# Optimization experiments

Measured on AMD Instinct MI355X. Metric: run time of the kernel, lower is better.

## Reference

```python
import jax, jax.numpy as jnp
import numpy as np
import math

DIM = 1024
NUM_HEADS = 16
HEAD_DIM = DIM // NUM_HEADS  # 64
BATCH = 4
SEQ = 4096


def setup_inputs() -> dict:
    key = jax.random.key(0)
    ks = jax.random.split(key, 10)
    s = 1.0 / math.sqrt(DIM)
    return {
        "x": jax.random.normal(ks[0], (BATCH, SEQ, DIM), dtype=jnp.float32),
        "Wq": jax.random.normal(ks[1], (DIM, DIM), dtype=jnp.float32) * s,
        "bq": jax.random.normal(ks[2], (DIM,), dtype=jnp.float32) * 0.01,
        "Wk": jax.random.normal(ks[3], (DIM, DIM), dtype=jnp.float32) * s,
        "bk": jax.random.normal(ks[4], (DIM,), dtype=jnp.float32) * 0.01,
        "Wv": jax.random.normal(ks[5], (DIM, DIM), dtype=jnp.float32) * s,
        "bv": jax.random.normal(ks[6], (DIM,), dtype=jnp.float32) * 0.01,
        "Wo": jax.random.normal(ks[7], (DIM, DIM), dtype=jnp.float32) * s,
        "bo": jax.random.normal(ks[8], (DIM,), dtype=jnp.float32) * 0.01,
        # Performer random projection buffer: randn * 0.4, [head_dim, feature_map_size]
        "R": jax.random.normal(ks[9], (HEAD_DIM, HEAD_DIM), dtype=jnp.float32) * 0.4,
    }


def _feature_map(x, R):
    # x: [b, h, n, d]; matches torch: x scaled first, then norm of scaled x
    x = x / math.sqrt(HEAD_DIM)
    proj = jnp.einsum("bhnd,dm->bhnm", x, R)
    sq_norm = jnp.sum(x * x, axis=-1, keepdims=True)  # ||x||^2
    return jnp.exp(proj - 0.5 * sq_norm)


def reference(x, Wq, bq, Wk, bk, Wv, bv, Wo, bo, R):
    b, n, _ = x.shape
    h, d = NUM_HEADS, HEAD_DIM

    def split_heads(t):
        return t.reshape(b, n, h, d).transpose(0, 2, 1, 3)  # [b,h,n,d]

    q = split_heads(x @ Wq.T + bq)
    k = split_heads(x @ Wk.T + bk)
    v = split_heads(x @ Wv.T + bv)

    q_prime = _feature_map(q, R)  # [b,h,n,m]
    k_prime = _feature_map(k, R)  # [b,h,n,m]

    kv = jnp.einsum("bhnd,bhne->bhde", k_prime, v)          # [b,h,m,d]
    z = 1.0 / (jnp.sum(q_prime, axis=-1) + 1e-8)            # [b,h,n]
    out = jnp.einsum("bhnd,bhde,bhn->bhne", q_prime, kv, z)  # [b,h,n,d]

    out = out.transpose(0, 2, 1, 3).reshape(b, n, DIM)
    return out @ Wo.T + bo
```

## Files before the change

### kernel.cpp

```cpp
#include <hip/hip_runtime.h>
#include <math.h>

#define DIM 1024
#define NH 16
#define HD 64
#define BATCH 4
#define SEQ 4096
#define NTOK (BATCH*SEQ)

typedef float f32x4 __attribute__((ext_vector_type(4)));
typedef short bf16x8 __attribute__((ext_vector_type(8)));

#define GLOAD_LDS16(gp, lp)                                                    \
  __builtin_amdgcn_global_load_lds(                                            \
      (const __attribute__((address_space(1))) unsigned int*)(gp),             \
      (__attribute__((address_space(3))) unsigned int*)(lp), 16, 0, 0)

__device__ __forceinline__ unsigned short f2bf(float f) {
  unsigned u = __float_as_uint(f);
  unsigned r = (u + 0x7fffu + ((u >> 16) & 1u)) >> 16;
  return (unsigned short)r;
}
__device__ __forceinline__ float bf2f(unsigned short s) {
  return __uint_as_float((unsigned)s << 16);
}

template <int NB_N, int OUT_BF16>
__global__ __launch_bounds__(256) void gemm_swz(
    const unsigned short* __restrict__ A,
    const unsigned short* __restrict__ B,
    const float* __restrict__ b0, const float* __restrict__ b1,
    const float* __restrict__ b2,
    void* __restrict__ C0, void* __restrict__ C1, void* __restrict__ C2)
{
    __shared__ unsigned short As[128 * 32];
    __shared__ unsigned short Bs[128 * 32];
    const int t    = threadIdx.x;
    const int lane = t & 63;
    const int w    = t >> 6;

    const int bid   = blockIdx.x;
    const int xcd   = bid & 7;
    const int local = bid >> 3;
    const int mi    = xcd * 16 + local / NB_N;
    const int ni    = local % NB_N;
    const int m0    = mi * 128;
    const int n0g   = ni * 128;

    const int wm = (w >> 1) * 64;
    const int wn = (w & 1) * 64;

    f32x4 acc[4][4] = {};

    const int srow = lane >> 2;
    const int sseg = ((lane & 3) ^ ((lane >> 3) & 3)) * 8;

    const int fr = lane & 15;
    const int q8 = lane >> 4;
    const int fq = (q8 ^ ((fr >> 1) & 3)) * 8;

    for (int k0 = 0; k0 < 1024; k0 += 32) {
#pragma unroll
        for (int i = 0; i < 2; i++) {
            int rbase = i * 64 + w * 16;
            GLOAD_LDS16(&A[(size_t)(m0 + rbase + srow) * 1024 + k0 + sseg],
                        &As[rbase * 32]);
            GLOAD_LDS16(&B[(size_t)(n0g + rbase + srow) * 1024 + k0 + sseg],
                        &Bs[rbase * 32]);
        }
        __syncthreads();

        bf16x8 af[4], bfr[4];
#pragma unroll
        for (int mt = 0; mt < 4; mt++)
            af[mt] = *(const bf16x8*)&As[(wm + mt * 16 + fr) * 32 + fq];
#pragma unroll
        for (int nt = 0; nt < 4; nt++)
            bfr[nt] = *(const bf16x8*)&Bs[(wn + nt * 16 + fr) * 32 + fq];
#pragma unroll
        for (int mt = 0; mt < 4; mt++)
#pragma unroll
            for (int nt = 0; nt < 4; nt++)
                acc[mt][nt] = __builtin_amdgcn_mfma_f32_16x16x32_bf16(
                    af[mt], bfr[nt], acc[mt][nt], 0, 0, 0);
        __syncthreads();
    }

    const int mat = ni >> 3;
    const float* bias = (NB_N == 8) ? b0 : (mat == 0 ? b0 : mat == 1 ? b1 : b2);
    void* Cp = (NB_N == 8) ? C0 : (mat == 0 ? C0 : mat == 1 ? C1 : C2);
    const int n0 = (ni & 7) * 128;

    const int col = lane & 15;
    const int rq  = (lane >> 4) * 4;
#pragma unroll
    for (int nt = 0; nt < 4; nt++) {
        int cbase = n0 + wn + nt * 16 + col;
        float bv = bias[cbase];
#pragma unroll
        for (int mt = 0; mt < 4; mt++) {
#pragma unroll
            for (int r = 0; r < 4; r++) {
                int row = m0 + wm + mt * 16 + rq + r;
                float val = acc[mt][nt][r] + bv;
                if (OUT_BF16)
                    ((unsigned short*)Cp)[(size_t)row * 1024 + cbase] = f2bf(val);
                else
                    ((float*)Cp)[(size_t)row * 1024 + cbase] = val;
            }
        }
    }
}

__global__ __launch_bounds__(256) void cast_bf16(
    const float* __restrict__ src, unsigned short* __restrict__ dst, int n)
{
    int i = (blockIdx.x * 256 + threadIdx.x) * 4;
    if (i >= n) return;
    float4 v = *(const float4*)&src[i];
    ushort2 lo = {f2bf(v.x), f2bf(v.y)};
    ushort2 hi = {f2bf(v.z), f2bf(v.w)};
    *(ushort2*)&dst[i] = lo;
    *(ushort2*)&dst[i + 2] = hi;
}

__global__ __launch_bounds__(256) void cast_bf16_w4(
    const float* __restrict__ s0, const float* __restrict__ s1,
    const float* __restrict__ s2, const float* __restrict__ s3,
    unsigned short* __restrict__ d0, unsigned short* __restrict__ d1,
    unsigned short* __restrict__ d2, unsigned short* __restrict__ d3)
{
    const float* s = (blockIdx.y == 0) ? s0 : (blockIdx.y == 1) ? s1
                    : (blockIdx.y == 2) ? s2 : s3;
    unsigned short* d = (blockIdx.y == 0) ? d0 : (blockIdx.y == 1) ? d1
                       : (blockIdx.y == 2) ? d2 : d3;
    int i = (blockIdx.x * 256 + threadIdx.x) * 4;
    float4 v = *(const float4*)&s[i];
    ushort2 lo = {f2bf(v.x), f2bf(v.y)};
    ushort2 hi = {f2bf(v.z), f2bf(v.w)};
    *(ushort2*)&d[i] = lo;
    *(ushort2*)&d[i + 2] = hi;
}

__global__ __launch_bounds__(256) void featmap_mfma(
    unsigned short* __restrict__ buf, const float* __restrict__ R)
{
    __shared__ unsigned short Rt[64 * 72];
    const int t = threadIdx.x;
    for (int i = t; i < 4096; i += 256) {
        int n = i >> 6, k = i & 63;
        Rt[n * 72 + k] = f2bf(R[k * 64 + n]);
    }
    __syncthreads();

    const int lane = t & 63;
    const int w = t >> 6;
    const size_t rowbase = (size_t)blockIdx.x * 256 + w * 64;
    const int fr = lane & 15;
    const int fq = (lane >> 4) * 8;

    f32x4 acc[4][4] = {};
    float sqacc[4] = {0.f, 0.f, 0.f, 0.f};

#pragma unroll
    for (int ks = 0; ks < 2; ks++) {
        bf16x8 bfr[4];
#pragma unroll
        for (int nt = 0; nt < 4; nt++)
            bfr[nt] = *(const bf16x8*)&Rt[(nt * 16 + fr) * 72 + ks * 32 + fq];
#pragma unroll
        for (int mt = 0; mt < 4; mt++) {
            bf16x8 a = *(const bf16x8*)
                &buf[(rowbase + mt * 16 + fr) * 64 + ks * 32 + fq];
#pragma unroll
            for (int j = 0; j < 8; j++) {
                float v = bf2f((unsigned short)a[j]);
                sqacc[mt] = fmaf(v, v, sqacc[mt]);
            }
#pragma unroll
            for (int nt = 0; nt < 4; nt++)
                acc[mt][nt] = __builtin_amdgcn_mfma_f32_16x16x32_bf16(
                    a, bfr[nt], acc[mt][nt], 0, 0, 0);
        }
    }
#pragma unroll
    for (int mt = 0; mt < 4; mt++) {
        sqacc[mt] += __shfl_xor(sqacc[mt], 16);
        sqacc[mt] += __shfl_xor(sqacc[mt], 32);
    }

    const int col = lane & 15;
    const int rq  = (lane >> 4) * 4;
#pragma unroll
    for (int mt = 0; mt < 4; mt++) {
#pragma unroll
        for (int r = 0; r < 4; r++) {
            float s = __shfl(sqacc[mt], rq + r);
            size_t row = rowbase + mt * 16 + rq + r;
#pragma unroll
            for (int nt = 0; nt < 4; nt++) {
                float val = acc[mt][nt][r] * 0.125f - s * 0.0078125f;
                buf[row * 64 + nt * 16 + col] = f2bf(__expf(val));
            }
        }
    }
}

__global__ __launch_bounds__(256) void kv_accum(
    const unsigned short* __restrict__ kp, const unsigned short* __restrict__ vp,
    float* __restrict__ kv)
{
    __shared__ float Ks[16][68];
    __shared__ float Vs[16][68];
    const int chunk = blockIdx.x;
    const int h = blockIdx.y;
    const int b = blockIdx.z;
    const int t = threadIdx.x;
    const int tx = t & 15, ty = t >> 4;
    float c[4][4] = {};
    const int nbase = b * SEQ + chunk * 512;
    const int nl = t >> 4, seg = t & 15;
    for (int n0 = 0; n0 < 512; n0 += 16) {
        size_t gaddr = (size_t)(nbase + n0 + nl) * DIM + h * 64 + seg * 4;
        ushort4 kq = *(const ushort4*)&kp[gaddr];
        ushort4 vq = *(const ushort4*)&vp[gaddr];
        Ks[nl][seg * 4 + 0] = bf2f(kq.x); Ks[nl][seg * 4 + 1] = bf2f(kq.y);
        Ks[nl][seg * 4 + 2] = bf2f(kq.z); Ks[nl][seg * 4 + 3] = bf2f(kq.w);
        Vs[nl][seg * 4 + 0] = bf2f(vq.x); Vs[nl][seg * 4 + 1] = bf2f(vq.y);
        Vs[nl][seg * 4 + 2] = bf2f(vq.z); Vs[nl][seg * 4 + 3] = bf2f(vq.w);
        __syncthreads();
#pragma unroll
        for (int nn = 0; nn < 16; nn++) {
            float4 a = *(const float4*)&Ks[nn][ty * 4];
            float4 bq = *(const float4*)&Vs[nn][tx * 4];
            float aa[4] = {a.x, a.y, a.z, a.w};
            float bb[4] = {bq.x, bq.y, bq.z, bq.w};
#pragma unroll
            for (int i = 0; i < 4; i++)
#pragma unroll
                for (int j = 0; j < 4; j++)
                    c[i][j] += aa[i] * bb[j];
        }
        __syncthreads();
    }
    float* dst = &kv[(size_t)(b * NH + h) * 64 * 64];
#pragma unroll
    for (int i = 0; i < 4; i++)
#pragma unroll
        for (int j = 0; j < 4; j++)
            atomicAdd(&dst[(ty * 4 + i) * 64 + tx * 4 + j], c[i][j]);
}

__global__ __launch_bounds__(256) void attn_out_mfma(
    const unsigned short* __restrict__ qp, const float* __restrict__ kv,
    unsigned short* __restrict__ ob)
{
    __shared__ unsigned short kvT[64 * 72];
    const int t = threadIdx.x;
    const int bh = blockIdx.y;
    const int b = bh >> 4, h = bh & 15;
    const float* kvp = &kv[(size_t)bh * 4096];
    for (int i = t; i < 4096; i += 256) {
        int m = i >> 6, e = i & 63;
        kvT[e * 72 + m] = f2bf(kvp[i]);
    }
    __syncthreads();

    const int lane = t & 63;
    const int w = t >> 6;
    const int rowInSeq = blockIdx.x * 256 + w * 64;
    const int fr = lane & 15;
    const int fq = (lane >> 4) * 8;

    f32x4 acc[4][4] = {};
    float rsum[4] = {0.f, 0.f, 0.f, 0.f};

#pragma unroll
    for (int ks = 0; ks < 2; ks++) {
        bf16x8 bfr[4];
#pragma unroll
        for (int nt = 0; nt < 4; nt++)
            bfr[nt] = *(const bf16x8*)&kvT[(nt * 16 + fr) * 72 + ks * 32 + fq];
#pragma unroll
        for (int mt = 0; mt < 4; mt++) {
            size_t n = (size_t)(b * SEQ + rowInSeq + mt * 16 + fr);
            bf16x8 a = *(const bf16x8*)&qp[n * DIM + h * 64 + ks * 32 + fq];
#pragma unroll
            for (int j = 0; j < 8; j++)
                rsum[mt] += bf2f((unsigned short)a[j]);
#pragma unroll
            for (int nt = 0; nt < 4; nt++)
                acc[mt][nt] = __builtin_amdgcn_mfma_f32_16x16x32_bf16(
                    a, bfr[nt], acc[mt][nt], 0, 0, 0);
        }
    }
#pragma unroll
    for (int mt = 0; mt < 4; mt++) {
        rsum[mt] += __shfl_xor(rsum[mt], 16);
        rsum[mt] += __shfl_xor(rsum[mt], 32);
    }

    const int col = lane & 15;
    const int rq  = (lane >> 4) * 4;
#pragma unroll
    for (int mt = 0; mt < 4; mt++) {
#pragma unroll
        for (int r = 0; r < 4; r++) {
            float s = __shfl(rsum[mt], rq + r);
            float z = 1.f / (s + 1e-8f);
            size_t n = (size_t)(b * SEQ + rowInSeq + mt * 16 + rq + r);
#pragma unroll
            for (int nt = 0; nt < 4; nt++)
                ob[n * DIM + h * 64 + nt * 16 + col] = f2bf(acc[mt][nt][r] * z);
        }
    }
}

extern "C" void kernel_launch(void* const* d_in, const int* in_sizes, int n_in,
                              void* d_out, int out_size, void* d_ws, size_t ws_size,
                              hipStream_t stream) {
    const float* x  = (const float*)d_in[0];
    const float* Wq = (const float*)d_in[1];
    const float* bq = (const float*)d_in[2];
    const float* Wk = (const float*)d_in[3];
    const float* bk = (const float*)d_in[4];
    const float* Wv = (const float*)d_in[5];
    const float* bv = (const float*)d_in[6];
    const float* Wo = (const float*)d_in[7];
    const float* bo = (const float*)d_in[8];
    const float* R  = (const float*)d_in[9];
    float* out = (float*)d_out;

    char* p = (char*)d_ws;
    unsigned short* xb = (unsigned short*)p; p += (size_t)NTOK * DIM * 2;
    unsigned short* qb = (unsigned short*)p; p += (size_t)NTOK * DIM * 2;
    unsigned short* kb = (unsigned short*)p; p += (size_t)NTOK * DIM * 2;
    unsigned short* vb = (unsigned short*)p; p += (size_t)NTOK * DIM * 2;
    float* kvb = (float*)p;                  p += (size_t)BATCH * NH * HD * HD * 4;
    unsigned short* wqkv = (unsigned short*)p; p += (size_t)3 * DIM * DIM * 2;
    unsigned short* wob  = (unsigned short*)p; p += (size_t)DIM * DIM * 2;

    hipMemsetAsync(kvb, 0, (size_t)BATCH * NH * HD * HD * sizeof(float), stream);

    cast_bf16<<<NTOK * DIM / (256 * 4), 256, 0, stream>>>(x, xb, NTOK * DIM);
    cast_bf16_w4<<<dim3(DIM * DIM / (256 * 4), 4), 256, 0, stream>>>(
        Wq, Wk, Wv, Wo,
        wqkv, wqkv + (size_t)DIM * DIM, wqkv + (size_t)2 * DIM * DIM, wob);

    gemm_swz<24, 1><<<3072, 256, 0, stream>>>(
        xb, wqkv, bq, bk, bv, qb, kb, vb);

    featmap_mfma<<<2 * NTOK * NH / 256, 256, 0, stream>>>(qb, R);

    kv_accum<<<dim3(8, NH, BATCH), 256, 0, stream>>>(kb, vb, kvb);

    attn_out_mfma<<<dim3(SEQ / 256, BATCH * NH), 256, 0, stream>>>(qb, kvb, xb);

    gemm_swz<8, 0><<<1024, 256, 0, stream>>>(
        xb, wob, bo, bo, bo, out, out, out);
}
```

Measured before the change: 419.4 us.

## Replace 128x128 GEMM with 256x256 tile, 4-stage async LDS pipeline

Rewrites both projection GEMMs to use 512-thread blocks computing 256x256 tiles, with a four-deep ring of LDS buffers filled by direct global-to-LDS loads issued three k-steps ahead. Barriers, waitcnt and setprio are placed by hand to overlap loads with MFMA work, and the block-index swizzle spreads tiles across XCDs. The goal is more reuse per tile and hidden memory latency; in exchange it uses 128KB of LDS per block, which limits occupancy, and the last GEMM runs as a single wave of blocks.

```diff
diff --git a/kernel.cpp b/kernel.cpp
--- a/kernel.cpp
+++ b/kernel.cpp
@@ -25,88 +25,134 @@
   return __uint_as_float((unsigned)s << 16);
 }
 
-template <int NB_N, int OUT_BF16>
-__global__ __launch_bounds__(256) void gemm_swz(
+template <int NT_N, int OUT_BF16>
+__global__ __launch_bounds__(512, 2) void gemm256(
     const unsigned short* __restrict__ A,
     const unsigned short* __restrict__ B,
     const float* __restrict__ b0, const float* __restrict__ b1,
     const float* __restrict__ b2,
     void* __restrict__ C0, void* __restrict__ C1, void* __restrict__ C2)
 {
-    __shared__ unsigned short As[128 * 32];
-    __shared__ unsigned short Bs[128 * 32];
+    __shared__ unsigned short lds[4][2][8192];
     const int t    = threadIdx.x;
     const int lane = t & 63;
     const int w    = t >> 6;
 
-    const int bid   = blockIdx.x;
-    const int xcd   = bid & 7;
-    const int local = bid >> 3;
-    const int mi    = xcd * 16 + local / NB_N;
-    const int ni    = local % NB_N;
-    const int m0    = mi * 128;
-    const int n0g   = ni * 128;
-
-    const int wm = (w >> 1) * 64;
-    const int wn = (w & 1) * 64;
-
-    f32x4 acc[4][4] = {};
-
-    const int srow = lane >> 2;
-    const int sseg = ((lane & 3) ^ ((lane >> 3) & 3)) * 8;
+    const int cpx = gridDim.x >> 3;
+    const int swz = (blockIdx.x & 7) * cpx + (blockIdx.x >> 3);
+    const int mi  = swz / NT_N;
+    const int ni  = swz % NT_N;
+    const int m0  = mi * 256;
+    const int n0g = ni * 256;
+
+    const int wm = (w >> 2) * 128;
+    const int wn = (w & 3) * 64;
+
+    const int srow = t >> 2;
+    const int sseg = ((t & 3) ^ ((t >> 3) & 3)) * 8;
+    const unsigned short* Ag = A + (size_t)(m0 + srow) * 1024 + sseg;
+    const unsigned short* Bg = B + (size_t)(n0g + srow) * 1024 + sseg;
+    const int ldst = w * 512;
 
     const int fr = lane & 15;
-    const int q8 = lane >> 4;
-    const int fq = (q8 ^ ((fr >> 1) & 3)) * 8;
-
-    for (int k0 = 0; k0 < 1024; k0 += 32) {
-#pragma unroll
-        for (int i = 0; i < 2; i++) {
-            int rbase = i * 64 + w * 16;
-            GLOAD_LDS16(&A[(size_t)(m0 + rbase + srow) * 1024 + k0 + sseg],
-                        &As[rbase * 32]);
-            GLOAD_LDS16(&B[(size_t)(n0g + rbase + srow) * 1024 + k0 + sseg],
-                        &Bs[rbase * 32]);
-        }
-        __syncthreads();
-
-        bf16x8 af[4], bfr[4];
-#pragma unroll
-        for (int mt = 0; mt < 4; mt++)
-            af[mt] = *(const bf16x8*)&As[(wm + mt * 16 + fr) * 32 + fq];
-#pragma unroll
-        for (int nt = 0; nt < 4; nt++)
-            bfr[nt] = *(const bf16x8*)&Bs[(wn + nt * 16 + fr) * 32 + fq];
-#pragma unroll
-        for (int mt = 0; mt < 4; mt++)
-#pragma unroll
-            for (int nt = 0; nt < 4; nt++)
-                acc[mt][nt] = __builtin_amdgcn_mfma_f32_16x16x32_bf16(
-                    af[mt], bfr[nt], acc[mt][nt], 0, 0, 0);
-        __syncthreads();
-    }
-
-    const int mat = ni >> 3;
-    const float* bias = (NB_N == 8) ? b0 : (mat == 0 ? b0 : mat == 1 ? b1 : b2);
-    void* Cp = (NB_N == 8) ? C0 : (mat == 0 ? C0 : mat == 1 ? C1 : C2);
-    const int n0 = (ni & 7) * 128;
+    const int fq = ((lane >> 4) ^ ((fr >> 1) & 3)) * 8;
+
+    f32x4 acc[8][4] = {};
+
+#define STAGE_A(hh, j)                                                        \
+  GLOAD_LDS16(Ag + (size_t)(j) * 131072 + (size_t)(hh) * 32,                  \
+              &lds[(hh) & 3][0][(j) * 4096 + ldst])
+#define STAGE_B(hh, j)                                                        \
+  GLOAD_LDS16(Bg + (size_t)(j) * 131072 + (size_t)(hh) * 32,                  \
+              &lds[(hh) & 3][1][(j) * 4096 + ldst])
+
+#define BOUNDARY(VM)                                                          \
+  asm volatile("s_waitcnt vmcnt(" #VM ")" ::: "memory");                      \
+  __builtin_amdgcn_s_barrier();                                               \
+  asm volatile("" ::: "memory");
+
+#define KHALF(h, DOSTAGE)                                                     \
+  {                                                                           \
+    const unsigned short* As_ = &lds[(h) & 3][0][0];                          \
+    const unsigned short* Bs_ = &lds[(h) & 3][1][0];                          \
+    bf16x8 bfr[4], afr[4];                                                    \
+    if (DOSTAGE) { STAGE_A((h) + 3, 0); STAGE_A((h) + 3, 1); }                \
+    _Pragma("unroll")                                                         \
+    for (int nf = 0; nf < 4; ++nf)                                            \
+      bfr[nf] = *(const bf16x8*)&Bs_[(wn + nf * 16 + fr) * 32 + fq];          \
+    _Pragma("unroll")                                                         \
+    for (int mf = 0; mf < 4; ++mf)                                            \
+      afr[mf] = *(const bf16x8*)&As_[(wm + mf * 16 + fr) * 32 + fq];          \
+    __builtin_amdgcn_s_barrier();                                             \
+    asm volatile("s_waitcnt lgkmcnt(0)" ::: "memory");                        \
+    __builtin_amdgcn_s_setprio(1);                                            \
+    _Pragma("unroll")                                                         \
+    for (int mf = 0; mf < 4; ++mf)                                            \
+      _Pragma("unroll")                                                       \
+      for (int nf = 0; nf < 4; ++nf)                                          \
+        acc[mf][nf] = __builtin_amdgcn_mfma_f32_16x16x32_bf16(                \
+            afr[mf], bfr[nf], acc[mf][nf], 0, 0, 0);                          \
+    __builtin_amdgcn_s_setprio(0);                                            \
+    __builtin_amdgcn_s_barrier();                                             \
+    asm volatile("" ::: "memory");                                            \
+    if (DOSTAGE) { STAGE_B((h) + 3, 0); STAGE_B((h) + 3, 1); }                \
+    _Pragma("unroll")                                                         \
+    for (int mf = 0; mf < 4; ++mf)                                            \
+      afr[mf] = *(const bf16x8*)&As_[(wm + 64 + mf * 16 + fr) * 32 + fq];     \
+    __builtin_amdgcn_s_barrier();                                             \
+    asm volatile("s_waitcnt lgkmcnt(0)" ::: "memory");                        \
+    __builtin_amdgcn_s_setprio(1);                                            \
+    _Pragma("unroll")                                                         \
+    for (int mf = 0; mf < 4; ++mf)                                            \
+      _Pragma("unroll")                                                       \
+      for (int nf = 0; nf < 4; ++nf)                                          \
+        acc[4 + mf][nf] = __builtin_amdgcn_mfma_f32_16x16x32_bf16(            \
+            afr[mf], bfr[nf], acc[4 + mf][nf], 0, 0, 0);                      \
+    __builtin_amdgcn_s_setprio(0);                                            \
+  }
+
+#pragma unroll
+    for (int hh = 0; hh < 3; ++hh) {
+        STAGE_A(hh, 0); STAGE_A(hh, 1);
+        STAGE_B(hh, 0); STAGE_B(hh, 1);
+    }
+
+#pragma unroll 1
+    for (int h = 0; h < 29; ++h) {
+        BOUNDARY(8);
+        KHALF(h, 1);
+    }
+    BOUNDARY(8); KHALF(29, 0);
+    BOUNDARY(4); KHALF(30, 0);
+    BOUNDARY(0); KHALF(31, 0);
+
+#undef KHALF
+#undef BOUNDARY
+#undef STAGE_A
+#undef STAGE_B
+
+    const int mat = ni >> 2;
+    const float* bias = (mat == 0) ? b0 : (mat == 1) ? b1 : b2;
+    void* Cp = (mat == 0) ? C0 : (mat == 1) ? C1 : C2;
+    const int n0 = (ni & 3) * 256;
 
     const int col = lane & 15;
     const int rq  = (lane >> 4) * 4;
 #pragma unroll
-    for (int nt = 0; nt < 4; nt++) {
-        int cbase = n0 + wn + nt * 16 + col;
+    for (int nf = 0; nf < 4; ++nf) {
+        int cbase = n0 + wn + nf * 16 + col;
         float bv = bias[cbase];
 #pragma unroll
-        for (int mt = 0; mt < 4; mt++) {
-#pragma unroll
-            for (int r = 0; r < 4; r++) {
-                int row = m0 + wm + mt * 16 + rq + r;
-                float val = acc[mt][nt][r] + bv;
+        for (int mf = 0; mf < 8; ++mf) {
+            int rbase = m0 + wm + (mf >> 2) * 64 + (mf & 3) * 16 + rq;
+#pragma unroll
+            for (int r = 0; r < 4; ++r) {
+                float val = acc[mf][nf][r] + bv;
+                size_t idx = (size_t)(rbase + r) * 1024 + cbase;
                 if (OUT_BF16)
-                    ((unsigned short*)Cp)[(size_t)row * 1024 + cbase] = f2bf(val);
+                    ((unsigned short*)Cp)[idx] = f2bf(val);
                 else
-                    ((float*)Cp)[(size_t)row * 1024 + cbase] = val;
+                    ((float*)Cp)[idx] = val;
             }
         }
     }
@@ -347,7 +393,7 @@
         Wq, Wk, Wv, Wo,
         wqkv, wqkv + (size_t)DIM * DIM, wqkv + (size_t)2 * DIM * DIM, wob);
 
-    gemm_swz<24, 1><<<3072, 256, 0, stream>>>(
+    gemm256<12, 1><<<768, 512, 0, stream>>>(
         xb, wqkv, bq, bk, bv, qb, kb, vb);
 
     featmap_mfma<<<2 * NTOK * NH / 256, 256, 0, stream>>>(qb, R);
@@ -356,6 +402,6 @@
 
     attn_out_mfma<<<dim3(SEQ / 256, BATCH * NH), 256, 0, stream>>>(qb, kvb, xb);
 
-    gemm_swz<8, 0><<<1024, 256, 0, stream>>>(
+    gemm256<4, 0><<<256, 512, 0, stream>>>(
         xb, wob, bo, bo, bo, out, out, out);
 }
```

Result: no change. 415.6 us (-0.9%).
